# Kernel tuning notes

Hardware: AMD Instinct MI355X
Metric: run time of the kernel (lower is better)

Reference implementation:

```python
import jax, jax.numpy as jnp
import numpy as np

EPS = 1e-6

def _diag_mul(w, z):
    # multiply by diag(exp(i*w))
    return jax.lax.complex(jnp.cos(w), jnp.sin(w)) * z

def _reflect(re, im, z):
    # z - (2/||v||^2) * (z @ conj(v)) outer v, v = re + i*im
    v = jax.lax.complex(re, im)                       # [N]
    sq_norm = jnp.sum(re * re + im * im)
    vz = jnp.einsum('bn,n->b', z, jnp.conj(v))        # [B]
    factor = 2.0 / sq_norm
    return z - (factor * vz)[:, None] * v[None, :]

def _mod_relu(z, bias):
    norm = jnp.abs(z)
    scale = jax.nn.relu(norm + bias) / (norm + EPS)   # real [B,N]
    return jax.lax.complex(jnp.real(z) * scale, jnp.imag(z) * scale)

def setup_inputs() -> dict:
    key = jax.random.key(0)
    ks = jax.random.split(key, 12)
    B, N_IN, N = 8192, 1024, 2048
    return {
        'inputs': jax.random.normal(ks[0], (B, N_IN), jnp.float32),
        'state': jax.random.normal(ks[1], (B, 2 * N), jnp.float32),
        'w_ih': jax.random.normal(ks[2], (2 * N, N_IN), jnp.float32) * (1.0 / np.sqrt(N_IN)),
        'b_h': jnp.zeros((N,), jnp.float32),
        'd1_w': jax.random.uniform(ks[3], (N,), jnp.float32, -np.pi, np.pi),
        'r1_re': jax.random.uniform(ks[4], (N,), jnp.float32, -1.0, 1.0),
        'r1_im': jax.random.uniform(ks[5], (N,), jnp.float32, -1.0, 1.0),
        'd2_w': jax.random.uniform(ks[6], (N,), jnp.float32, -np.pi, np.pi),
        'r2_re': jax.random.uniform(ks[7], (N,), jnp.float32, -1.0, 1.0),
        'r2_im': jax.random.uniform(ks[8], (N,), jnp.float32, -1.0, 1.0),
        'd3_w': jax.random.uniform(ks[9], (N,), jnp.float32, -np.pi, np.pi),
        'perm': jax.random.permutation(ks[10], N).astype(jnp.int32),
    }

def reference(inputs, state, w_ih, b_h, d1_w, r1_re, r1_im, d2_w, r2_re, r2_im, d3_w, perm):
    N = b_h.shape[0]
    # input projection then split into complex
    inputs_mul = inputs @ w_ih.T                                  # [B, 2N]
    inputs_c = jax.lax.complex(inputs_mul[:, :N], inputs_mul[:, N:])
    state_c = jax.lax.complex(state[:, :N], state[:, N:])
    z = _diag_mul(d1_w, state_c)
    z = jnp.fft.fft(z, axis=-1)
    z = _reflect(r1_re, r1_im, z)
    z = z[:, perm]                                                # permutation of hidden dim
    z = _diag_mul(d2_w, z)
    z = jnp.fft.ifft(z, axis=-1)
    z = _reflect(r2_re, r2_im, z)
    z = _diag_mul(d3_w, z)
    preact = inputs_c + z
    new_c = _mod_relu(preact, b_h)
    new_state = jnp.concatenate([jnp.real(new_c), jnp.imag(new_c)], axis=1)
    return new_state
```

## Files before the change

kernel.cpp:

```cpp
#include <hip/hip_runtime.h>
#include <hip/hip_bf16.h>

#define GLOBAL_AS __attribute__((address_space(1)))
#define LDS_AS    __attribute__((address_space(3)))

typedef __bf16 bf16x8 __attribute__((ext_vector_type(8)));
typedef float  f32x4  __attribute__((ext_vector_type(4)));
typedef unsigned short u16x8 __attribute__((ext_vector_type(8)));
typedef LDS_AS float ldsf_t;

#define BATCH  8192
#define KDIM   1024
#define NDIM   4096
#define NHALF  2048
#define KTILES 32

__device__ __forceinline__ unsigned short bf16_rne(float f) {
  unsigned int u = __float_as_uint(f);
  u += 0x7fffu + ((u >> 16) & 1u);
  return (unsigned short)(u >> 16);
}
__device__ __forceinline__ float bf16_f32(unsigned short h) {
  return __uint_as_float(((unsigned int)h) << 16);
}

__global__ __launch_bounds__(256) void cvt_split(const float* __restrict__ src,
                                                 unsigned short* __restrict__ dst,
                                                 int rows) {
  int i = blockIdx.x * 256 + threadIdx.x;
  if (i >= rows * 128) return;
  int m = i >> 7, c = i & 127;
  const float4* s4 = (const float4*)(src + ((size_t)m * KDIM + c * 8));
  float4 x0 = s4[0], x1 = s4[1];
  float xs[8] = {x0.x, x0.y, x0.z, x0.w, x1.x, x1.y, x1.z, x1.w};
  u16x8 hv, lv;
#pragma unroll
  for (int j = 0; j < 8; ++j) {
    unsigned short h = bf16_rne(xs[j]);
    hv[j] = h;
    lv[j] = bf16_rne(xs[j] - bf16_f32(h));
  }
  size_t base = ((size_t)m * KTILES + (c >> 2)) * 64 + (size_t)(c & 3) * 8;
  *(u16x8*)(dst + base) = hv;
  *(u16x8*)(dst + base + 32) = lv;
}

__global__ __launch_bounds__(256) void tables_kernel(
    const float* __restrict__ d1, const float* __restrict__ r1re, const float* __restrict__ r1im,
    const float* __restrict__ d2, const float* __restrict__ r2re, const float* __restrict__ r2im,
    const float* __restrict__ d3, float* __restrict__ T) {
  __shared__ float red[8];
  int tid = threadIdx.x;
  const float invN = 1.0f / 2048.0f;
  for (int j = tid; j < NHALF; j += 256) {
    float s, c;
    sincosf(d1[j], &s, &c); T[j] = c;            T[2048 + j] = s;
    sincosf(d2[j], &s, &c); T[4096 + j] = c * invN; T[6144 + j] = s * invN;
    sincosf(d3[j], &s, &c); T[8192 + j] = c;     T[10240 + j] = s;
  }
  float n1 = 0.f, n2 = 0.f;
  for (int j = tid; j < NHALF; j += 256) {
    n1 += r1re[j] * r1re[j] + r1im[j] * r1im[j];
    n2 += r2re[j] * r2re[j] + r2im[j] * r2im[j];
  }
#pragma unroll
  for (int off = 32; off; off >>= 1) {
    n1 += __shfl_down(n1, off);
    n2 += __shfl_down(n2, off);
  }
  if ((tid & 63) == 0) { red[(tid >> 6) * 2] = n1; red[(tid >> 6) * 2 + 1] = n2; }
  __syncthreads();
  if (tid == 0) {
    T[12288] = 2.0f / (red[0] + red[2] + red[4] + red[6]);
    T[12289] = 2.0f / (red[1] + red[3] + red[5] + red[7]);
  }
}

__global__ __launch_bounds__(256) void gemm_split(const unsigned short* __restrict__ Acvt,
                                                  const unsigned short* __restrict__ Wcvt,
                                                  float* __restrict__ C) {
  __shared__ __attribute__((aligned(16))) unsigned short sA[128 * 64];
  __shared__ __attribute__((aligned(16))) unsigned short sW[128 * 64];

  int bid = blockIdx.x;
  int swz = (bid & 7) * 256 + (bid >> 3);
  int bm = swz >> 5;
  int bn = swz & 31;

  int tid = threadIdx.x;
  int w = tid >> 6, l = tid & 63;
  int wr = w >> 1, wc = w & 1;
  int g = l >> 4;

  f32x4 acc[4][4] = {};

#pragma unroll 1
  for (int kt = 0; kt < KTILES; ++kt) {
    __syncthreads();
#pragma unroll
    for (int i = 0; i < 4; ++i) {
      int rgrp = (w * 4 + i) * 8;
      int row = rgrp + (l >> 3);
      int chunk = (l & 7) ^ (l >> 3);
      const unsigned short* srcA = Acvt + (((size_t)(bm * 128 + row)) * KTILES + kt) * 64 + chunk * 8;
      const unsigned short* srcW = Wcvt + (((size_t)(bn * 128 + row)) * KTILES + kt) * 64 + chunk * 8;
      __builtin_amdgcn_global_load_lds((GLOBAL_AS const void*)srcA, (LDS_AS void*)(sA + rgrp * 64), 16, 0, 0);
      __builtin_amdgcn_global_load_lds((GLOBAL_AS const void*)srcW, (LDS_AS void*)(sW + rgrp * 64), 16, 0, 0);
    }
    __syncthreads();

    bf16x8 a_hi[4], a_lo[4], b_hi[4], b_lo[4];
#pragma unroll
    for (int mi = 0; mi < 4; ++mi) {
      int row = wr * 64 + mi * 16 + (l & 15);
      int ph = g ^ (row & 7);
      a_hi[mi] = *(const bf16x8*)&sA[row * 64 + ph * 8];
      a_lo[mi] = *(const bf16x8*)&sA[row * 64 + (ph ^ 4) * 8];
    }
#pragma unroll
    for (int ni = 0; ni < 4; ++ni) {
      int row = wc * 64 + ni * 16 + (l & 15);
      int ph = g ^ (row & 7);
      b_hi[ni] = *(const bf16x8*)&sW[row * 64 + ph * 8];
      b_lo[ni] = *(const bf16x8*)&sW[row * 64 + (ph ^ 4) * 8];
    }
#pragma unroll
    for (int mi = 0; mi < 4; ++mi)
#pragma unroll
      for (int ni = 0; ni < 4; ++ni) {
        acc[mi][ni] = __builtin_amdgcn_mfma_f32_16x16x32_bf16(a_hi[mi], b_hi[ni], acc[mi][ni], 0, 0, 0);
        acc[mi][ni] = __builtin_amdgcn_mfma_f32_16x16x32_bf16(a_hi[mi], b_lo[ni], acc[mi][ni], 0, 0, 0);
        acc[mi][ni] = __builtin_amdgcn_mfma_f32_16x16x32_bf16(a_lo[mi], b_hi[ni], acc[mi][ni], 0, 0, 0);
      }
  }

  int r0 = bm * 128 + wr * 64 + g * 4;
  int c0 = bn * 128 + wc * 64 + (l & 15);
#pragma unroll
  for (int mi = 0; mi < 4; ++mi)
#pragma unroll
    for (int ni = 0; ni < 4; ++ni)
#pragma unroll
      for (int i = 0; i < 4; ++i)
        C[(size_t)(r0 + mi * 16 + i) * NDIM + (c0 + ni * 16)] = acc[mi][ni][i];
}

__device__ __forceinline__ void fft_stages(ldsf_t*& sr, ldsf_t*& si, ldsf_t*& dr, ldsf_t*& di,
                                           const ldsf_t* Wc, const ldsf_t* Ws, int tid, float sgn) {
  int s = 1;
#pragma unroll 1
  for (int stage = 0; stage < 11; ++stage) {
    int smask = s - 1;
#pragma unroll
    for (int tt = 0; tt < 4; ++tt) {
      int t = tid + tt * 256;
      int q = t & smask;
      int k = t - q;
      float ar = sr[t], ai = si[t];
      float br = sr[t + 1024], bi = si[t + 1024];
      float wr = Wc[k], wi = sgn * Ws[k];
      float er = ar + br, ei = ai + bi;
      float fr = ar - br, fi = ai - bi;
      int j0 = t + k;
      dr[j0] = er;             di[j0] = ei;
      dr[j0 + s] = fr * wr - fi * wi;
      di[j0 + s] = fr * wi + fi * wr;
    }
    ldsf_t* tp = sr; sr = dr; dr = tp;
    tp = si; si = di; di = tp;
    s <<= 1;
    __syncthreads();
  }
}

__device__ __forceinline__ void reflect_inplace(ldsf_t* zr, ldsf_t* zi,
                                                const float* __restrict__ vre_g,
                                                const float* __restrict__ vim_g,
                                                float fac, ldsf_t* red, int tid) {
  float vr[8], vi[8], zre[8], zim[8];
  float ar = 0.f, ai = 0.f;
#pragma unroll
  for (int jj = 0; jj < 8; ++jj) {
    int j = tid + jj * 256;
    vr[jj] = vre_g[j]; vi[jj] = vim_g[j];
    zre[jj] = zr[j];   zim[jj] = zi[j];
    ar += zre[jj] * vr[jj] + zim[jj] * vi[jj];
    ai += zim[jj] * vr[jj] - zre[jj] * vi[jj];
  }
#pragma unroll
  for (int off = 32; off; off >>= 1) {
    ar += __shfl_down(ar, off);
    ai += __shfl_down(ai, off);
  }
  if ((tid & 63) == 0) { red[(tid >> 6) * 2] = ar; red[(tid >> 6) * 2 + 1] = ai; }
  __syncthreads();
  float vzr = red[0] + red[2] + red[4] + red[6];
  float vzi = red[1] + red[3] + red[5] + red[7];
  __syncthreads();
  float cr = fac * vzr, ci = fac * vzi;
#pragma unroll
  for (int jj = 0; jj < 8; ++jj) {
    int j = tid + jj * 256;
    zr[j] = zre[jj] - (cr * vr[jj] - ci * vi[jj]);
    zi[j] = zim[jj] - (cr * vi[jj] + ci * vr[jj]);
  }
}

__global__ __launch_bounds__(256) void urnn_z(
    const float* __restrict__ state, const float* __restrict__ imul,
    const float* __restrict__ T,
    const float* __restrict__ r1re, const float* __restrict__ r1im,
    const float* __restrict__ r2re, const float* __restrict__ r2im,
    const float* __restrict__ bh, const int* __restrict__ perm,
    float* __restrict__ out) {
  __shared__ float Xre[2048], Xim[2048], Yre[2048], Yim[2048];
  __shared__ float Wc_s[1024], Ws_s[1024];
  __shared__ float red_s[8];

  const int r = blockIdx.x, tid = threadIdx.x;
  const float fac1 = T[12288], fac2 = T[12289];

  ldsf_t* Xr = (ldsf_t*)Xre; ldsf_t* Xi = (ldsf_t*)Xim;
  ldsf_t* Yr = (ldsf_t*)Yre; ldsf_t* Yi = (ldsf_t*)Yim;
  ldsf_t* Wc = (ldsf_t*)Wc_s; ldsf_t* Ws = (ldsf_t*)Ws_s;
  ldsf_t* red = (ldsf_t*)red_s;

  for (int k = tid; k < 1024; k += 256) {
    float s, c;
    sincosf(-6.28318530717958647692f * ((float)k * (1.0f / 2048.0f)), &s, &c);
    Wc[k] = c; Ws[k] = s;
  }

  const float* srow = state + (size_t)r * NDIM;
#pragma unroll
  for (int jj = 0; jj < 8; ++jj) {
    int j = tid + jj * 256;
    float re = srow[j], im = srow[j + NHALF];
    float c = T[j], s = T[2048 + j];
    Xr[j] = re * c - im * s;
    Xi[j] = re * s + im * c;
  }
  __syncthreads();

  ldsf_t *sr = Xr, *si = Xi, *dr = Yr, *di = Yi;

  fft_stages(sr, si, dr, di, Wc, Ws, tid, 1.0f);
  reflect_inplace(sr, si, r1re, r1im, fac1, red, tid);
  __syncthreads();

#pragma unroll
  for (int jj = 0; jj < 8; ++jj) {
    int j = tid + jj * 256;
    int idx = perm[j];
    float zr = sr[idx], zi = si[idx];
    float c = T[4096 + j], s = T[6144 + j];
    dr[j] = zr * c - zi * s;
    di[j] = zr * s + zi * c;
  }
  __syncthreads();
  { ldsf_t* tp = sr; sr = dr; dr = tp; tp = si; si = di; di = tp; }

  fft_stages(sr, si, dr, di, Wc, Ws, tid, -1.0f);
  reflect_inplace(sr, si, r2re, r2im, fac2, red, tid);

  const float* irow = imul + (size_t)r * NDIM;
  float* orow = out + (size_t)r * NDIM;
#pragma unroll
  for (int jj = 0; jj < 8; ++jj) {
    int j = tid + jj * 256;
    float c3 = T[8192 + j], s3 = T[10240 + j];
    float zre = sr[j], zim = si[j];
    float pr = irow[j] + (zre * c3 - zim * s3);
    float pi = irow[j + NHALF] + (zre * s3 + zim * c3);
    float norm = sqrtf(pr * pr + pi * pi);
    float scale = fmaxf(norm + bh[j], 0.0f) / (norm + 1e-6f);
    orow[j] = pr * scale;
    orow[j + NHALF] = pi * scale;
  }
}

extern "C" void kernel_launch(void* const* d_in, const int* in_sizes, int n_in,
                              void* d_out, int out_size, void* d_ws, size_t ws_size,
                              hipStream_t stream) {
  const float* inputs = (const float*)d_in[0];
  const float* state  = (const float*)d_in[1];
  const float* w_ih   = (const float*)d_in[2];
  const float* b_h    = (const float*)d_in[3];
  const float* d1_w   = (const float*)d_in[4];
  const float* r1_re  = (const float*)d_in[5];
  const float* r1_im  = (const float*)d_in[6];
  const float* d2_w   = (const float*)d_in[7];
  const float* r2_re  = (const float*)d_in[8];
  const float* r2_im  = (const float*)d_in[9];
  const float* d3_w   = (const float*)d_in[10];
  const int*   perm   = (const int*)d_in[11];
  float* out = (float*)d_out;
  (void)in_sizes; (void)n_in; (void)out_size; (void)ws_size;

  char* ws = (char*)d_ws;
  float*          imul = (float*)(ws);
  unsigned short* Acvt = (unsigned short*)(ws + 134217728ull);
  unsigned short* Wcvt = (unsigned short*)(ws + 134217728ull + 33554432ull);
  float*          T    = (float*)(ws + 134217728ull + 33554432ull + 16777216ull);

  cvt_split<<<4096, 256, 0, stream>>>(inputs, Acvt, BATCH);
  cvt_split<<<2048, 256, 0, stream>>>(w_ih, Wcvt, NDIM);
  tables_kernel<<<1, 256, 0, stream>>>(d1_w, r1_re, r1_im, d2_w, r2_re, r2_im, d3_w, T);
  gemm_split<<<2048, 256, 0, stream>>>(Acvt, Wcvt, imul);
  urnn_z<<<BATCH, 256, 0, stream>>>(state, imul, T, r1_re, r1_im, r2_re, r2_im, b_h, perm, out);
}
```

Baseline: 643.1 us.

## Replace radix-2 LDS FFT with radix-8 Stockham stages and swizzled float2 LDS

Rewrites the per-row 2048-point FFT from eleven radix-2 stages with split re/im arrays into three radix-8 stages plus a final radix-4 stage. Data is held as interleaved float2 with an XOR swizzle to reduce bank conflicts, and the last stage leaves results in registers so the reflection is applied without an LDS round trip. This cuts barrier count and LDS traffic roughly fourfold and raises occupancy via launch_bounds(256,4) with a smaller LDS footprint. The cost is more registers and twiddles recomputed by complex multiplication, which can lose a little precision.

After: 586.0 us. 8.9% less time.

```diff
diff --git a/kernel.cpp b/kernel.cpp
--- a/kernel.cpp
+++ b/kernel.cpp
@@ -7,7 +7,6 @@
 typedef __bf16 bf16x8 __attribute__((ext_vector_type(8)));
 typedef float  f32x4  __attribute__((ext_vector_type(4)));
 typedef unsigned short u16x8 __attribute__((ext_vector_type(8)));
-typedef LDS_AS float ldsf_t;
 
 #define BATCH  8192
 #define KDIM   1024
@@ -145,137 +144,192 @@
         C[(size_t)(r0 + mi * 16 + i) * NDIM + (c0 + ni * 16)] = acc[mi][ni][i];
 }
 
-__device__ __forceinline__ void fft_stages(ldsf_t*& sr, ldsf_t*& si, ldsf_t*& dr, ldsf_t*& di,
-                                           const ldsf_t* Wc, const ldsf_t* Ws, int tid, float sgn) {
-  int s = 1;
-#pragma unroll 1
-  for (int stage = 0; stage < 11; ++stage) {
-    int smask = s - 1;
-#pragma unroll
-    for (int tt = 0; tt < 4; ++tt) {
-      int t = tid + tt * 256;
-      int q = t & smask;
-      int k = t - q;
-      float ar = sr[t], ai = si[t];
-      float br = sr[t + 1024], bi = si[t + 1024];
-      float wr = Wc[k], wi = sgn * Ws[k];
-      float er = ar + br, ei = ai + bi;
-      float fr = ar - br, fi = ai - bi;
-      int j0 = t + k;
-      dr[j0] = er;             di[j0] = ei;
-      dr[j0 + s] = fr * wr - fi * wi;
-      di[j0 + s] = fr * wi + fi * wr;
-    }
-    ldsf_t* tp = sr; sr = dr; dr = tp;
-    tp = si; si = di; di = tp;
-    s <<= 1;
-    __syncthreads();
-  }
-}
-
-__device__ __forceinline__ void reflect_inplace(ldsf_t* zr, ldsf_t* zi,
-                                                const float* __restrict__ vre_g,
-                                                const float* __restrict__ vim_g,
-                                                float fac, ldsf_t* red, int tid) {
-  float vr[8], vi[8], zre[8], zim[8];
+__device__ __forceinline__ int SW(int i) { return i ^ ((i >> 4) & 15); }
+
+__device__ __forceinline__ float2 cmul(float2 a, float2 b) {
+  return make_float2(a.x * b.x - a.y * b.y, a.x * b.y + a.y * b.x);
+}
+
+template<int SGN>
+__device__ __forceinline__ void dft8(const float2 a[8], float2 X[8]) {
+  const float Sf = (float)SGN;
+  float t0r = a[0].x + a[4].x, t0i = a[0].y + a[4].y;
+  float t2r = a[0].x - a[4].x, t2i = a[0].y - a[4].y;
+  float t1r = a[2].x + a[6].x, t1i = a[2].y + a[6].y;
+  float t3r = a[2].x - a[6].x, t3i = a[2].y - a[6].y;
+  float E0r = t0r + t1r, E0i = t0i + t1i, E2r = t0r - t1r, E2i = t0i - t1i;
+  float E1r = t2r - Sf * t3i, E1i = t2i + Sf * t3r;
+  float E3r = t2r + Sf * t3i, E3i = t2i - Sf * t3r;
+  float s0r = a[1].x + a[5].x, s0i = a[1].y + a[5].y;
+  float s2r = a[1].x - a[5].x, s2i = a[1].y - a[5].y;
+  float s1r = a[3].x + a[7].x, s1i = a[3].y + a[7].y;
+  float s3r = a[3].x - a[7].x, s3i = a[3].y - a[7].y;
+  float O0r = s0r + s1r, O0i = s0i + s1i, O2r = s0r - s1r, O2i = s0i - s1i;
+  float O1r = s2r - Sf * s3i, O1i = s2i + Sf * s3r;
+  float O3r = s2r + Sf * s3i, O3i = s2i - Sf * s3r;
+  const float C2 = 0.70710678118654752440f;
+  float u0r = O0r, u0i = O0i;
+  float u1r = C2 * (O1r - Sf * O1i), u1i = C2 * (O1i + Sf * O1r);
+  float u2r = -Sf * O2i, u2i = Sf * O2r;
+  float u3r = -C2 * (O3r + Sf * O3i), u3i = C2 * (Sf * O3r - O3i);
+  X[0] = make_float2(E0r + u0r, E0i + u0i); X[4] = make_float2(E0r - u0r, E0i - u0i);
+  X[1] = make_float2(E1r + u1r, E1i + u1i); X[5] = make_float2(E1r - u1r, E1i - u1i);
+  X[2] = make_float2(E2r + u2r, E2i + u2i); X[6] = make_float2(E2r - u2r, E2i - u2i);
+  X[3] = make_float2(E3r + u3r, E3i + u3i); X[7] = make_float2(E3r - u3r, E3i - u3i);
+}
+
+template<int SGN, int S>
+__device__ __forceinline__ void radix8_wr(const float2 a[8], float2* dst, const float2* Tw, int t) {
+  float2 X[8];
+  dft8<SGN>(a, X);
+  int q = t & (S - 1);
+  int ps = t - q;
+  float2 tw = Tw[ps];
+  float2 w1 = make_float2(tw.x, (SGN < 0) ? tw.y : -tw.y);
+  float2 w2 = cmul(w1, w1), w3 = cmul(w2, w1), w4 = cmul(w2, w2);
+  float2 w5 = cmul(w4, w1), w6 = cmul(w4, w2), w7 = cmul(w4, w3);
+  int base = 8 * ps + q;
+  dst[SW(base)]         = X[0];
+  dst[SW(base + S)]     = cmul(X[1], w1);
+  dst[SW(base + 2 * S)] = cmul(X[2], w2);
+  dst[SW(base + 3 * S)] = cmul(X[3], w3);
+  dst[SW(base + 4 * S)] = cmul(X[4], w4);
+  dst[SW(base + 5 * S)] = cmul(X[5], w5);
+  dst[SW(base + 6 * S)] = cmul(X[6], w6);
+  dst[SW(base + 7 * S)] = cmul(X[7], w7);
+}
+
+template<int SGN, int S>
+__device__ __forceinline__ void radix8_ld(const float2* src, float2* dst, const float2* Tw, int t) {
+  float2 a[8];
+#pragma unroll
+  for (int j = 0; j < 8; ++j) a[j] = src[SW(t + 256 * j)];
+  radix8_wr<SGN, S>(a, dst, Tw, t);
+}
+
+template<int SGN>
+__device__ __forceinline__ void radix4_final(const float2* src, float2 z[8], int t) {
+  const float Sf = (float)SGN;
+#pragma unroll
+  for (int h = 0; h < 2; ++h) {
+    int q = t + 256 * h;
+    float2 a0 = src[SW(q)], a1 = src[SW(q + 512)], a2 = src[SW(q + 1024)], a3 = src[SW(q + 1536)];
+    float t0r = a0.x + a2.x, t0i = a0.y + a2.y, t2r = a0.x - a2.x, t2i = a0.y - a2.y;
+    float t1r = a1.x + a3.x, t1i = a1.y + a3.y, t3r = a1.x - a3.x, t3i = a1.y - a3.y;
+    z[0 + h] = make_float2(t0r + t1r, t0i + t1i);
+    z[4 + h] = make_float2(t0r - t1r, t0i - t1i);
+    z[2 + h] = make_float2(t2r - Sf * t3i, t2i + Sf * t3r);
+    z[6 + h] = make_float2(t2r + Sf * t3i, t2i - Sf * t3r);
+  }
+}
+
+__device__ __forceinline__ void reflect_reg(float2 z[8],
+                                            const float* __restrict__ vre,
+                                            const float* __restrict__ vim,
+                                            float fac, volatile float* red, int t) {
+  float vr[8], vi[8];
   float ar = 0.f, ai = 0.f;
 #pragma unroll
-  for (int jj = 0; jj < 8; ++jj) {
-    int j = tid + jj * 256;
-    vr[jj] = vre_g[j]; vi[jj] = vim_g[j];
-    zre[jj] = zr[j];   zim[jj] = zi[j];
-    ar += zre[jj] * vr[jj] + zim[jj] * vi[jj];
-    ai += zim[jj] * vr[jj] - zre[jj] * vi[jj];
+  for (int j = 0; j < 8; ++j) {
+    int o = t + 256 * j;
+    vr[j] = vre[o]; vi[j] = vim[o];
+    ar += z[j].x * vr[j] + z[j].y * vi[j];
+    ai += z[j].y * vr[j] - z[j].x * vi[j];
   }
 #pragma unroll
   for (int off = 32; off; off >>= 1) {
     ar += __shfl_down(ar, off);
     ai += __shfl_down(ai, off);
   }
-  if ((tid & 63) == 0) { red[(tid >> 6) * 2] = ar; red[(tid >> 6) * 2 + 1] = ai; }
+  int w = t >> 6;
+  if ((t & 63) == 0) { red[w * 2] = ar; red[w * 2 + 1] = ai; }
   __syncthreads();
   float vzr = red[0] + red[2] + red[4] + red[6];
   float vzi = red[1] + red[3] + red[5] + red[7];
   __syncthreads();
   float cr = fac * vzr, ci = fac * vzi;
 #pragma unroll
-  for (int jj = 0; jj < 8; ++jj) {
-    int j = tid + jj * 256;
-    zr[j] = zre[jj] - (cr * vr[jj] - ci * vi[jj]);
-    zi[j] = zim[jj] - (cr * vi[jj] + ci * vr[jj]);
-  }
-}
-
-__global__ __launch_bounds__(256) void urnn_z(
+  for (int j = 0; j < 8; ++j) {
+    z[j].x -= cr * vr[j] - ci * vi[j];
+    z[j].y -= cr * vi[j] + ci * vr[j];
+  }
+}
+
+__global__ __launch_bounds__(256, 4) void urnn_z(
     const float* __restrict__ state, const float* __restrict__ imul,
     const float* __restrict__ T,
     const float* __restrict__ r1re, const float* __restrict__ r1im,
     const float* __restrict__ r2re, const float* __restrict__ r2im,
     const float* __restrict__ bh, const int* __restrict__ perm,
     float* __restrict__ out) {
-  __shared__ float Xre[2048], Xim[2048], Yre[2048], Yim[2048];
-  __shared__ float Wc_s[1024], Ws_s[1024];
-  __shared__ float red_s[8];
-
-  const int r = blockIdx.x, tid = threadIdx.x;
+  __shared__ __attribute__((aligned(16))) float2 Abuf[2048];
+  __shared__ __attribute__((aligned(16))) float2 Bbuf[2048];
+  __shared__ __attribute__((aligned(16))) float2 Tw[256];
+  __shared__ float red[8];
+
+  const int t = threadIdx.x, r = blockIdx.x;
   const float fac1 = T[12288], fac2 = T[12289];
 
-  ldsf_t* Xr = (ldsf_t*)Xre; ldsf_t* Xi = (ldsf_t*)Xim;
-  ldsf_t* Yr = (ldsf_t*)Yre; ldsf_t* Yi = (ldsf_t*)Yim;
-  ldsf_t* Wc = (ldsf_t*)Wc_s; ldsf_t* Ws = (ldsf_t*)Ws_s;
-  ldsf_t* red = (ldsf_t*)red_s;
-
-  for (int k = tid; k < 1024; k += 256) {
-    float s, c;
-    sincosf(-6.28318530717958647692f * ((float)k * (1.0f / 2048.0f)), &s, &c);
-    Wc[k] = c; Ws[k] = s;
+  {
+    float sn, cs;
+    sincosf(-6.28318530717958647692f * ((float)t * (1.0f / 2048.0f)), &sn, &cs);
+    Tw[t] = make_float2(cs, sn);
   }
 
   const float* srow = state + (size_t)r * NDIM;
-#pragma unroll
-  for (int jj = 0; jj < 8; ++jj) {
-    int j = tid + jj * 256;
-    float re = srow[j], im = srow[j + NHALF];
-    float c = T[j], s = T[2048 + j];
-    Xr[j] = re * c - im * s;
-    Xi[j] = re * s + im * c;
-  }
-  __syncthreads();
-
-  ldsf_t *sr = Xr, *si = Xi, *dr = Yr, *di = Yi;
-
-  fft_stages(sr, si, dr, di, Wc, Ws, tid, 1.0f);
-  reflect_inplace(sr, si, r1re, r1im, fac1, red, tid);
-  __syncthreads();
-
-#pragma unroll
-  for (int jj = 0; jj < 8; ++jj) {
-    int j = tid + jj * 256;
-    int idx = perm[j];
-    float zr = sr[idx], zi = si[idx];
-    float c = T[4096 + j], s = T[6144 + j];
-    dr[j] = zr * c - zi * s;
-    di[j] = zr * s + zi * c;
-  }
-  __syncthreads();
-  { ldsf_t* tp = sr; sr = dr; dr = tp; tp = si; si = di; di = tp; }
-
-  fft_stages(sr, si, dr, di, Wc, Ws, tid, -1.0f);
-  reflect_inplace(sr, si, r2re, r2im, fac2, red, tid);
+  float2 a[8];
+#pragma unroll
+  for (int j = 0; j < 8; ++j) {
+    int o = t + 256 * j;
+    float re = srow[o], im = srow[o + NHALF];
+    float c = T[o], s = T[2048 + o];
+    a[j] = make_float2(re * c - im * s, re * s + im * c);
+  }
+  radix8_wr<-1, 1>(a, Abuf, Tw, t);
+  __syncthreads();
+  radix8_ld<-1, 8>(Abuf, Bbuf, Tw, t);
+  __syncthreads();
+  radix8_ld<-1, 64>(Bbuf, Abuf, Tw, t);
+  __syncthreads();
+  float2 z[8];
+  radix4_final<-1>(Abuf, z, t);
+
+  reflect_reg(z, r1re, r1im, fac1, red, t);
+
+#pragma unroll
+  for (int j = 0; j < 8; ++j) Bbuf[SW(t + 256 * j)] = z[j];
+  __syncthreads();
+
+#pragma unroll
+  for (int j = 0; j < 8; ++j) {
+    int o = t + 256 * j;
+    int pp = perm[o];
+    float2 zz = Bbuf[SW(pp)];
+    float c = T[4096 + o], s = T[6144 + o];
+    a[j] = make_float2(zz.x * c - zz.y * s, zz.x * s + zz.y * c);
+  }
+  radix8_wr<+1, 1>(a, Abuf, Tw, t);
+  __syncthreads();
+  radix8_ld<+1, 8>(Abuf, Bbuf, Tw, t);
+  __syncthreads();
+  radix8_ld<+1, 64>(Bbuf, Abuf, Tw, t);
+  __syncthreads();
+  radix4_final<+1>(Abuf, z, t);
+
+  reflect_reg(z, r2re, r2im, fac2, red, t);
 
   const float* irow = imul + (size_t)r * NDIM;
   float* orow = out + (size_t)r * NDIM;
 #pragma unroll
-  for (int jj = 0; jj < 8; ++jj) {
-    int j = tid + jj * 256;
-    float c3 = T[8192 + j], s3 = T[10240 + j];
-    float zre = sr[j], zim = si[j];
-    float pr = irow[j] + (zre * c3 - zim * s3);
-    float pi = irow[j + NHALF] + (zre * s3 + zim * c3);
+  for (int j = 0; j < 8; ++j) {
+    int o = t + 256 * j;
+    float c3 = T[8192 + o], s3 = T[10240 + o];
+    float pr = irow[o] + (z[j].x * c3 - z[j].y * s3);
+    float pi = irow[o + NHALF] + (z[j].x * s3 + z[j].y * c3);
     float norm = sqrtf(pr * pr + pi * pi);
-    float scale = fmaxf(norm + bh[j], 0.0f) / (norm + 1e-6f);
-    orow[j] = pr * scale;
-    orow[j + NHALF] = pi * scale;
+    float scale = fmaxf(norm + bh[o], 0.0f) / (norm + 1e-6f);
+    orow[o] = pr * scale;
+    orow[o + NHALF] = pi * scale;
   }
 }
 
```
